# Kernel tuning notes

Hardware: AMD Instinct MI355X
Metric: run time of the kernel (lower is better)

Reference implementation:

```python
import jax, jax.numpy as jnp
import numpy as np
from jax import lax

SPARSITY = 0.5  # args.sparsity: fraction of weights KEPT


def get_subnet(scores, k):
    """GetSubnet.forward: sort |scores|, zero lowest (1-k) fraction, one elsewhere."""
    sa = jnp.abs(scores)
    n = sa.size
    j = int((1.0 - k) * n)  # static: number of entries zeroed
    idx = jnp.argsort(sa.ravel())  # ascending, matches torch .sort()
    mask = jnp.zeros((n,), dtype=sa.dtype).at[idx[j:]].set(1.0)
    return mask.reshape(scores.shape)


def masked_conv(x, w, s, b, stride):
    m = get_subnet(s, SPARSITY)
    y = lax.conv_general_dilated(
        x, w * m, window_strides=(stride, stride), padding=((1, 1), (1, 1)),
        dimension_numbers=('NCHW', 'OIHW', 'NCHW'))
    return y + b[None, :, None, None]


def setup_inputs() -> dict:
    key = jax.random.key(0)
    ks = jax.random.split(key, 16)
    def rn(k, shape, scale):
        return jax.random.normal(k, shape, dtype=jnp.float32) * scale
    return {
        'x':   rn(ks[0], (64, 3, 64, 64), 1.0),
        'w1':  rn(ks[1], (128, 3, 3, 3), 0.2),   's1': rn(ks[2], (128, 3, 3, 3), 1.0),   'b1': rn(ks[3], (128,), 0.01),
        'w2':  rn(ks[4], (256, 128, 3, 3), 0.05), 's2': rn(ks[5], (256, 128, 3, 3), 1.0), 'b2': rn(ks[6], (256,), 0.01),
        'w3':  rn(ks[7], (512, 256, 3, 3), 0.03), 's3': rn(ks[8], (512, 256, 3, 3), 1.0), 'b3': rn(ks[9], (512,), 0.01),
        'fw1': rn(ks[10], (1024, 512), 0.05),     'fs1': rn(ks[11], (1024, 512), 1.0),    'fb1': rn(ks[12], (1024,), 0.01),
        'fw2': rn(ks[13], (10, 1024), 0.05),      'fs2': rn(ks[14], (10, 1024), 1.0),     'fb2': rn(ks[15], (10,), 0.01),
    }


def reference(x, w1, s1, b1, w2, s2, b2, w3, s3, b3, fw1, fs1, fb1, fw2, fs2, fb2):
    h = jax.nn.relu(masked_conv(x, w1, s1, b1, stride=1))   # [64,128,64,64]
    h = jax.nn.relu(masked_conv(h, w2, s2, b2, stride=2))   # [64,256,32,32]
    h = jax.nn.relu(masked_conv(h, w3, s3, b3, stride=2))   # [64,512,16,16]
    h = h.mean(axis=(2, 3))                                 # [64,512] global avg pool
    m1 = get_subnet(fs1, SPARSITY)
    h = jax.nn.relu(h @ (fw1 * m1).T + fb1)                 # [64,1024]
    m2 = get_subnet(fs2, SPARSITY)
    return h @ (fw2 * m2).T + fb2                           # [64,10]
```

## Files before the change

### kernel.cpp

```cpp
#include <hip/hip_runtime.h>
#include <stdint.h>


typedef __attribute__((ext_vector_type(8))) short short8;
typedef __attribute__((ext_vector_type(4))) short short4v;
typedef __attribute__((ext_vector_type(4))) float floatx4;

__device__ __forceinline__ unsigned short f2bf(float f) {
    unsigned u = __float_as_uint(f);
    u += 0x7fffu + ((u >> 16) & 1u);
    return (unsigned short)(u >> 16);
}

constexpr unsigned CUM0 = 3456u;
constexpr unsigned CUM1 = 298368u;
constexpr unsigned CUM2 = 1478016u;
constexpr unsigned CUM3 = 2002304u;
constexpr unsigned STOT = 2012544u;
constexpr int NBH = 512;

__device__ __forceinline__ int find_tensor(unsigned idx, unsigned& li) {
    if (idx < CUM0) { li = idx;        return 0; }
    if (idx < CUM1) { li = idx - CUM0; return 1; }
    if (idx < CUM2) { li = idx - CUM1; return 2; }
    if (idx < CUM3) { li = idx - CUM2; return 3; }
    li = idx - CUM3; return 4;
}

__global__ __launch_bounds__(256) void hist11(const float* __restrict__ s0,
                                              const float* __restrict__ s1,
                                              const float* __restrict__ s2,
                                              const float* __restrict__ s3,
                                              const float* __restrict__ s4,
                                              const unsigned* __restrict__ P,
                                              unsigned* __restrict__ ghist, int pass) {
    __shared__ unsigned lh[10240];
    const int tid = threadIdx.x;
    const int NB = (pass == 2) ? 512 : 2048;
    for (int i = tid; i < NB * 5; i += 256) lh[i] = 0;
    __syncthreads();

    unsigned pref[5];
    #pragma unroll
    for (int t = 0; t < 5; t++) pref[t] = pass ? P[t] : 0u;
    const int fsh = (pass == 1) ? 20 : 9;

    for (unsigned idx = blockIdx.x * 256u + tid; idx < STOT; idx += NBH * 256u) {
        unsigned li; int t = find_tensor(idx, li);
        const float* sp = t == 0 ? s0 : t == 1 ? s1 : t == 2 ? s2 : t == 3 ? s3 : s4;
        unsigned key = __float_as_uint(sp[li]) & 0x7fffffffu;
        bool ok = (pass == 0) || ((key >> fsh) == pref[t]);
        if (ok) {
            unsigned bin = (pass == 0) ? (key >> 20)
                         : (pass == 1) ? ((key >> 9) & 2047u)
                                       : (key & 511u);
            atomicAdd(&lh[(unsigned)t * NB + bin], 1u);
        }
    }
    __syncthreads();
    const int goff = (pass == 0) ? 0 : (pass == 1) ? 10240 : 20480;
    for (int i = tid; i < NB * 5; i += 256) {
        unsigned v = lh[i];
        if (v) atomicAdd(&ghist[goff + i], v);
    }
}

__global__ __launch_bounds__(256) void find11(const unsigned* __restrict__ ghist,
                                              unsigned* __restrict__ P,
                                              unsigned* __restrict__ targ, int pass) {
    const int t = blockIdx.x;
    const int tid = threadIdx.x;
    const int NB = (pass == 2) ? 512 : 2048;
    const int goff = (pass == 0) ? 0 : (pass == 1) ? 10240 : 20480;
    const int seg = NB / 256;
    __shared__ unsigned bins[2048];
    __shared__ unsigned part[256];
    for (int i = tid; i < NB; i += 256) bins[i] = ghist[goff + t * NB + i];
    __syncthreads();
    unsigned s = 0;
    for (int j = 0; j < seg; j++) s += bins[tid * seg + j];
    part[tid] = s;
    __syncthreads();
    if (tid == 0) {
        unsigned n = t == 0 ? 3456u : t == 1 ? 294912u : t == 2 ? 1179648u
                   : t == 3 ? 524288u : 10240u;
        unsigned target = (pass == 0) ? (n >> 1) : targ[t];
        unsigned cum = 0; int q = 0;
        for (; q < 256; q++) { unsigned c = part[q]; if (cum + c > target) break; cum += c; }
        int b = q * seg;
        for (;; b++) { unsigned c = bins[b]; if (cum + c > target) break; cum += c; }
        targ[t] = target - cum;
        if (pass == 0)      P[t] = (unsigned)b;
        else if (pass == 1) P[t] = (P[t] << 11) | (unsigned)b;
        else                P[t] = (P[t] << 9) | (unsigned)b;
    }
}

__global__ void mask_reorder(const float* __restrict__ w0, const float* __restrict__ w1,
                             const float* __restrict__ w2, const float* __restrict__ w3,
                             const float* __restrict__ w4,
                             const float* __restrict__ s0, const float* __restrict__ s1,
                             const float* __restrict__ s2, const float* __restrict__ s3,
                             const float* __restrict__ s4,
                             const unsigned* __restrict__ T,
                             float* __restrict__ wm1,
                             unsigned short* __restrict__ A2,
                             unsigned short* __restrict__ A3,
                             float* __restrict__ fwm1, float* __restrict__ fwm2,
                             float* __restrict__ pooled) {
    unsigned idx = blockIdx.x * 256u + threadIdx.x;
    if (idx >= STOT) return;
    if (idx < 32768u) pooled[idx] = 0.f;
    unsigned li; int t = find_tensor(idx, li);
    const float* sp = t == 0 ? s0 : t == 1 ? s1 : t == 2 ? s2 : t == 3 ? s3 : s4;
    const float* wp = t == 0 ? w0 : t == 1 ? w1 : t == 2 ? w2 : t == 3 ? w3 : w4;
    unsigned key = __float_as_uint(sp[li]) & 0x7fffffffu;
    float val = (key >= T[t]) ? wp[li] : 0.f;
    if (t == 0) {
        wm1[li] = val;
    } else if (t == 1) {
        unsigned k = li / 1152u, r = li - k * 1152u;
        unsigned c = r / 9u, e = r - c * 9u;
        A2[((size_t)e * 256u + k) * 128u + c] = f2bf(val);
    } else if (t == 2) {
        unsigned k = li / 2304u, r = li - k * 2304u;
        unsigned c = r / 9u, e = r - c * 9u;
        A3[((size_t)e * 512u + k) * 256u + c] = f2bf(val);
    } else if (t == 3) {
        fwm1[li] = val;
    } else {
        fwm2[li] = val;
    }
}

template <int C, int H, int W, int K, int TX, int TY, int KT>
__global__ __launch_bounds__(TX* TY) void conv_direct(const float* __restrict__ in,
                                                      const float* __restrict__ wm,
                                                      const float* __restrict__ bias,
                                                      unsigned short* __restrict__ out) {
    constexpr int TILW = TX * 2, TILH = TY * 2;
    constexpr int ITW = TILW + 2, ITH = TILH + 2;
    constexpr int NTHREADS = TX * TY;
    constexpr int NLOAD = (ITH * ITW + NTHREADS - 1) / NTHREADS;
    constexpr int KG = K / KT;

    __shared__ float sIn[ITH * ITW];
    __shared__ float sW[9 * KT];

    const int tid = threadIdx.x;
    const int tx = tid % TX, ty = tid / TX;
    const int kg = blockIdx.z % KG, n = blockIdx.z / KG;
    const int ox0 = blockIdx.x * TILW, oy0 = blockIdx.y * TILH;
    const int ix0 = ox0 - 1, iy0 = oy0 - 1;

    const float* inN = in + (size_t)n * C * H * W;
    const float* wkg = wm + (size_t)kg * KT * C * 9;

    int goff[NLOAD];
    #pragma unroll
    for (int i = 0; i < NLOAD; i++) {
        int idx = tid + i * NTHREADS;
        if (idx < ITH * ITW) {
            int r = idx / ITW, col = idx % ITW;
            int gy = iy0 + r, gx = ix0 + col;
            goff[i] = (gy >= 0 && gy < H && gx >= 0 && gx < W) ? (gy * W + gx) : -1;
        } else goff[i] = -2;
    }

    float acc[2][2][KT];
    #pragma unroll
    for (int py = 0; py < 2; py++)
        #pragma unroll
        for (int px = 0; px < 2; px++)
            #pragma unroll
            for (int j = 0; j < KT; j++) acc[py][px][j] = 0.f;

    for (int c = 0; c < C; c++) {
        const float* inC = inN + (size_t)c * H * W;
        #pragma unroll
        for (int i = 0; i < NLOAD; i++) {
            int g = goff[i];
            if (g >= -1) sIn[tid + i * NTHREADS] = (g >= 0) ? inC[g] : 0.f;
        }
        for (int i = tid; i < 9 * KT; i += NTHREADS) {
            int e = i / KT, j = i % KT;
            sW[i] = wkg[j * C * 9 + c * 9 + e];
        }
        __syncthreads();

        float vin[4][4];
        const float* base = &sIn[(ty * 2) * ITW + tx * 2];
        #pragma unroll
        for (int r = 0; r < 4; r++)
            #pragma unroll
            for (int cc = 0; cc < 4; cc++) vin[r][cc] = base[r * ITW + cc];

        #pragma unroll
        for (int e = 0; e < 9; e++) {
            const int dy = e / 3, dx = e % 3;
            #pragma unroll
            for (int j = 0; j < KT; j++) {
                float wv = sW[e * KT + j];
                #pragma unroll
                for (int py = 0; py < 2; py++)
                    #pragma unroll
                    for (int px = 0; px < 2; px++)
                        acc[py][px][j] = fmaf(vin[py + dy][px + dx], wv, acc[py][px][j]);
            }
        }
        __syncthreads();
    }

    float bj[KT];
    #pragma unroll
    for (int j = 0; j < KT; j++) bj[j] = bias[kg * KT + j];
    #pragma unroll
    for (int py = 0; py < 2; py++)
        #pragma unroll
        for (int px = 0; px < 2; px++) {
            int oy = oy0 + ty * 2 + py, ox = ox0 + tx * 2 + px;
            short8 v;
            #pragma unroll
            for (int j = 0; j < KT; j++) {
                float t = acc[py][px][j] + bj[j];
                v[j] = (short)f2bf(t > 0.f ? t : 0.f);
            }
            *(short8*)(out + ((size_t)(n * H + oy) * W + ox) * K + kg * KT) = v;
        }
}

template <int C, int H, int W, int KOUT, bool POOL>
__global__ __launch_bounds__(256) void conv_mfma(const unsigned short* __restrict__ in,
                                                 const unsigned short* __restrict__ A,
                                                 const float* __restrict__ bias,
                                                 void* __restrict__ outv) {
    constexpr int OH = H / 2, OW = W / 2;
    constexpr int PR = 128 / OW;
    constexpr int RH = 2 * PR + 1;
    constexpr int IW = W + 1;
    constexpr int NC = C / 32;
    constexpr int PSTR = 40;
    constexpr int NSLOT = RH * IW * 4;
    constexpr int SLMAX = (NSLOT + 255) / 256;

    __shared__ unsigned short sIn[RH * IW * PSTR];

    const int tid = threadIdx.x;
    const int lane = tid & 63;
    const int wv = tid >> 6;
    const int l15 = lane & 15;
    const int quad = lane >> 4;
    const int pt = blockIdx.x, kb = blockIdx.y, n = blockIdx.z;
    const int k0 = kb * 128;
    const int oy0 = pt * PR;
    const int g0y = 2 * oy0 - 1;
    const int mw = wv * 32;

    int goff[SLMAX], slds[SLMAX];
    #pragma unroll
    for (int i = 0; i < SLMAX; i++) {
        int s = tid + i * 256;
        if (s < NSLOT) {
            int q = s & 3, pix = s >> 2;
            int ix = pix % IW, iy = pix / IW;
            int gy = g0y + iy, gx = ix - 1;
            slds[i] = pix * PSTR + q * 8;
            goff[i] = (gy >= 0 && gy < H && gx >= 0) ? ((gy * W + gx) * C + q * 8) : -1;
        } else { goff[i] = -2; slds[i] = 0; }
    }

    int pB[8];
    #pragma unroll
    for (int fn = 0; fn < 8; fn++) {
        int p = fn * 16 + l15;
        int oyl = p / OW, oxl = p % OW;
        pB[fn] = (oyl * 2 * IW + oxl * 2) * PSTR + quad * 8;
    }

    const unsigned short* inN = in + (size_t)n * H * W * C;

    floatx4 acc[2][8];
    #pragma unroll
    for (int fm = 0; fm < 2; fm++)
        #pragma unroll
        for (int fn = 0; fn < 8; fn++) acc[fm][fn] = (floatx4){0.f, 0.f, 0.f, 0.f};

    for (int cc = 0; cc < NC; cc++) {
        __syncthreads();
        const int cof = cc * 32;
        #pragma unroll
        for (int i = 0; i < SLMAX; i++) {
            int g = goff[i];
            if (g >= 0) {
                *(short8*)&sIn[slds[i]] = *(const short8*)(inN + g + cof);
            } else if (g == -1 && cc == 0) {
                *(short8*)&sIn[slds[i]] = (short8){0, 0, 0, 0, 0, 0, 0, 0};
            }
        }
        __syncthreads();

        const unsigned short* Abase = A + (size_t)(k0 + mw + l15) * C + cof + quad * 8;
        const size_t estr = (size_t)KOUT * C;

        short8 a0 = *(const short8*)(Abase);
        short8 a1 = *(const short8*)(Abase + 16 * C);

        #pragma unroll 1
        for (int e = 0; e < 9; e++) {
            short8 ac0 = a0, ac1 = a1;
            if (e < 8) {
                a0 = *(const short8*)(Abase + (size_t)(e + 1) * estr);
                a1 = *(const short8*)(Abase + (size_t)(e + 1) * estr + 16 * C);
            }
            const int dy = e / 3, dx = e - dy * 3;
            const int boff = (dy * IW + dx) * PSTR;
            short8 bfr[8];
            #pragma unroll
            for (int fn = 0; fn < 8; fn++)
                bfr[fn] = *(const short8*)&sIn[pB[fn] + boff];
            #pragma unroll
            for (int fn = 0; fn < 8; fn++) {
                acc[0][fn] = __builtin_amdgcn_mfma_f32_16x16x32_bf16(ac0, bfr[fn], acc[0][fn], 0, 0, 0);
                acc[1][fn] = __builtin_amdgcn_mfma_f32_16x16x32_bf16(ac1, bfr[fn], acc[1][fn], 0, 0, 0);
            }
        }
    }

    if (!POOL) {
        unsigned short* out = (unsigned short*)outv;
        #pragma unroll
        for (int fm = 0; fm < 2; fm++) {
            const int k4 = k0 + mw + fm * 16 + quad * 4;
            float b0 = bias[k4], b1 = bias[k4 + 1], b2 = bias[k4 + 2], b3 = bias[k4 + 3];
            #pragma unroll
            for (int fn = 0; fn < 8; fn++) {
                int p = fn * 16 + l15;
                int oy = oy0 + p / OW, ox = p % OW;
                float v0 = acc[fm][fn][0] + b0, v1 = acc[fm][fn][1] + b1;
                float v2 = acc[fm][fn][2] + b2, v3 = acc[fm][fn][3] + b3;
                short4v v;
                v[0] = (short)f2bf(v0 > 0.f ? v0 : 0.f);
                v[1] = (short)f2bf(v1 > 0.f ? v1 : 0.f);
                v[2] = (short)f2bf(v2 > 0.f ? v2 : 0.f);
                v[3] = (short)f2bf(v3 > 0.f ? v3 : 0.f);
                *(short4v*)(out + ((size_t)(n * OH + oy) * OW + ox) * KOUT + k4) = v;
            }
        }
    } else {
        float* out = (float*)outv;
        #pragma unroll
        for (int fm = 0; fm < 2; fm++) {
            #pragma unroll
            for (int reg = 0; reg < 4; reg++) {
                int k = k0 + mw + fm * 16 + quad * 4 + reg;
                float bv = bias[k];
                float s = 0.f;
                #pragma unroll
                for (int fn = 0; fn < 8; fn++) {
                    float v = acc[fm][fn][reg] + bv;
                    s += v > 0.f ? v : 0.f;
                }
                s += __shfl_xor(s, 1); s += __shfl_xor(s, 2);
                s += __shfl_xor(s, 4); s += __shfl_xor(s, 8);
                if (l15 == 0) atomicAdd(&out[n * KOUT + k], s * (1.0f / (OH * OW)));
            }
        }
    }
}

__global__ void fc1_kernel(const float* __restrict__ pooled, const float* __restrict__ w,
                           const float* __restrict__ b, float* __restrict__ out) {
    int t = blockIdx.x * 256 + threadIdx.x;
    int o = t & 1023, n = t >> 10;
    const float4* w4 = (const float4*)(w + (size_t)o * 512);
    const float4* p4 = (const float4*)(pooled + (size_t)n * 512);
    float acc = 0.f;
    for (int i = 0; i < 128; i++) {
        float4 a = p4[i], ww = w4[i];
        acc += a.x * ww.x + a.y * ww.y + a.z * ww.z + a.w * ww.w;
    }
    acc += b[o];
    out[t] = acc > 0.f ? acc : 0.f;
}

__global__ void fc2_kernel(const float* __restrict__ h, const float* __restrict__ w,
                           const float* __restrict__ b, float* __restrict__ out) {
    int n = blockIdx.x, tid = threadIdx.x;
    __shared__ float redw[40];
    const float4* h4 = (const float4*)(h + (size_t)n * 1024);
    float4 a = h4[tid];
    for (int o = 0; o < 10; o++) {
        const float4* w4 = (const float4*)(w + (size_t)o * 1024);
        float4 ww = w4[tid];
        float v = a.x * ww.x + a.y * ww.y + a.z * ww.z + a.w * ww.w;
        for (int off = 32; off > 0; off >>= 1) v += __shfl_down(v, off);
        if ((tid & 63) == 0) redw[o * 4 + (tid >> 6)] = v;
    }
    __syncthreads();
    if (tid < 10) {
        float s = redw[tid * 4] + redw[tid * 4 + 1] + redw[tid * 4 + 2] + redw[tid * 4 + 3] + b[tid];
        out[n * 10 + tid] = s;
    }
}

extern "C" void kernel_launch(void* const* d_in, const int* in_sizes, int n_in,
                              void* d_out, int out_size, void* d_ws, size_t ws_size,
                              hipStream_t stream) {
    const float* x   = (const float*)d_in[0];
    const float* w1  = (const float*)d_in[1];
    const float* s1  = (const float*)d_in[2];
    const float* b1  = (const float*)d_in[3];
    const float* w2  = (const float*)d_in[4];
    const float* s2  = (const float*)d_in[5];
    const float* b2  = (const float*)d_in[6];
    const float* w3  = (const float*)d_in[7];
    const float* s3  = (const float*)d_in[8];
    const float* b3  = (const float*)d_in[9];
    const float* fw1 = (const float*)d_in[10];
    const float* fs1 = (const float*)d_in[11];
    const float* fb1 = (const float*)d_in[12];
    const float* fw2 = (const float*)d_in[13];
    const float* fs2 = (const float*)d_in[14];
    const float* fb2 = (const float*)d_in[15];
    float* out = (float*)d_out;

    char* ws = (char*)d_ws;
    size_t off = 0;
    auto alloc = [&](size_t bytes) -> char* {
        char* p = ws + off;
        off = (off + bytes + 255) & ~(size_t)255;
        return p;
    };
    unsigned* ghist = (unsigned*)alloc(23040ull * 4);
    unsigned* P     = (unsigned*)alloc(64);
    unsigned* targ  = (unsigned*)alloc(64);
    float* wm1  = (float*)alloc(3456ull * 4);
    float* fwm1 = (float*)alloc(524288ull * 4);
    float* fwm2 = (float*)alloc(10240ull * 4);
    unsigned short* A2 = (unsigned short*)alloc(294912ull * 2);
    unsigned short* A3 = (unsigned short*)alloc(1179648ull * 2);
    unsigned short* h1 = (unsigned short*)alloc(33554432ull * 2);
    unsigned short* h2 = (unsigned short*)alloc(16777216ull * 2);
    float* pooled = (float*)alloc(32768ull * 4);
    float* fc1h   = (float*)alloc(65536ull * 4);
    if (off > ws_size) return;

    (void)hipMemsetAsync(ghist, 0, 23040ull * 4, stream);

    for (int pass = 0; pass < 3; pass++) {
        hist11<<<NBH, 256, 0, stream>>>(s1, s2, s3, fs1, fs2, P, ghist, pass);
        find11<<<5, 256, 0, stream>>>(ghist, P, targ, pass);
    }
    int gs = (STOT + 255) / 256;
    mask_reorder<<<gs, 256, 0, stream>>>(w1, w2, w3, fw1, fw2, s1, s2, s3, fs1, fs2, P,
                                         wm1, A2, A3, fwm1, fwm2, pooled);

    conv_direct<3, 64, 64, 128, 16, 16, 8>
        <<<dim3(2, 2, 64 * 16), 256, 0, stream>>>(x, wm1, b1, h1);
    conv_mfma<128, 64, 64, 256, false>
        <<<dim3(8, 2, 64), 256, 0, stream>>>(h1, A2, b2, h2);
    conv_mfma<256, 32, 32, 512, true>
        <<<dim3(2, 4, 64), 256, 0, stream>>>(h2, A3, b3, pooled);

    fc1_kernel<<<256, 256, 0, stream>>>(pooled, fwm1, fb1, fc1h);
    fc2_kernel<<<64, 256, 0, stream>>>(fc1h, fwm2, fb2, out);
}
```

Measured before the change: 403.1 us.

## Prefetch conv input chunks into registers and shrink MFMA pixel tiles

The two MFMA conv kernels now load the next channel chunk from global memory into registers while the current chunk is computed from shared memory. This hides global load latency behind the MFMA work. The pixel tile per block is halved from 128 to 64, which doubles the grid and cuts accumulator registers, and launch bounds now request 4 blocks per SM. Layer 3 also swaps the grid's y and z axes to change block scheduling order. The costs are an extra barrier per chunk, more register staging, and weight fragments reloaded across twice as many blocks.

```diff
diff --git a/kernel.cpp b/kernel.cpp
--- a/kernel.cpp
+++ b/kernel.cpp
@@ -229,13 +229,14 @@
         }
 }
 
-template <int C, int H, int W, int KOUT, bool POOL>
-__global__ __launch_bounds__(256) void conv_mfma(const unsigned short* __restrict__ in,
-                                                 const unsigned short* __restrict__ A,
-                                                 const float* __restrict__ bias,
-                                                 void* __restrict__ outv) {
+template <int C, int H, int W, int KOUT, int NPIX, bool POOL, bool SWAPYZ>
+__global__ __launch_bounds__(256, 4) void conv_mfma(const unsigned short* __restrict__ in,
+                                                    const unsigned short* __restrict__ A,
+                                                    const float* __restrict__ bias,
+                                                    void* __restrict__ outv) {
     constexpr int OH = H / 2, OW = W / 2;
-    constexpr int PR = 128 / OW;
+    constexpr int PR = NPIX / OW;
+    constexpr int FN = NPIX / 16;
     constexpr int RH = 2 * PR + 1;
     constexpr int IW = W + 1;
     constexpr int NC = C / 32;
@@ -250,7 +251,9 @@
     const int wv = tid >> 6;
     const int l15 = lane & 15;
     const int quad = lane >> 4;
-    const int pt = blockIdx.x, kb = blockIdx.y, n = blockIdx.z;
+    const int pt = blockIdx.x;
+    const int kb = SWAPYZ ? blockIdx.z : blockIdx.y;
+    const int n  = SWAPYZ ? blockIdx.y : blockIdx.z;
     const int k0 = kb * 128;
     const int oy0 = pt * PR;
     const int g0y = 2 * oy0 - 1;
@@ -269,9 +272,9 @@
         } else { goff[i] = -2; slds[i] = 0; }
     }
 
-    int pB[8];
-    #pragma unroll
-    for (int fn = 0; fn < 8; fn++) {
+    int pB[FN];
+    #pragma unroll
+    for (int fn = 0; fn < FN; fn++) {
         int p = fn * 16 + l15;
         int oyl = p / OW, oxl = p % OW;
         pB[fn] = (oyl * 2 * IW + oxl * 2) * PSTR + quad * 8;
@@ -279,25 +282,39 @@
 
     const unsigned short* inN = in + (size_t)n * H * W * C;
 
-    floatx4 acc[2][8];
+    floatx4 acc[2][FN];
     #pragma unroll
     for (int fm = 0; fm < 2; fm++)
         #pragma unroll
-        for (int fn = 0; fn < 8; fn++) acc[fm][fn] = (floatx4){0.f, 0.f, 0.f, 0.f};
+        for (int fn = 0; fn < FN; fn++) acc[fm][fn] = (floatx4){0.f, 0.f, 0.f, 0.f};
+
+    short8 st[SLMAX];
+    #pragma unroll
+    for (int i = 0; i < SLMAX; i++) {
+        int g = goff[i];
+        if (g >= 0) st[i] = *(const short8*)(inN + g);
+    }
 
     for (int cc = 0; cc < NC; cc++) {
-        __syncthreads();
         const int cof = cc * 32;
         #pragma unroll
         for (int i = 0; i < SLMAX; i++) {
             int g = goff[i];
             if (g >= 0) {
-                *(short8*)&sIn[slds[i]] = *(const short8*)(inN + g + cof);
+                *(short8*)&sIn[slds[i]] = st[i];
             } else if (g == -1 && cc == 0) {
                 *(short8*)&sIn[slds[i]] = (short8){0, 0, 0, 0, 0, 0, 0, 0};
             }
         }
         __syncthreads();
+        if (cc + 1 < NC) {
+            const int ncof = cof + 32;
+            #pragma unroll
+            for (int i = 0; i < SLMAX; i++) {
+                int g = goff[i];
+                if (g >= 0) st[i] = *(const short8*)(inN + g + ncof);
+            }
+        }
 
         const unsigned short* Abase = A + (size_t)(k0 + mw + l15) * C + cof + quad * 8;
         const size_t estr = (size_t)KOUT * C;
@@ -314,16 +331,17 @@
             }
             const int dy = e / 3, dx = e - dy * 3;
             const int boff = (dy * IW + dx) * PSTR;
-            short8 bfr[8];
-            #pragma unroll
-            for (int fn = 0; fn < 8; fn++)
+            short8 bfr[FN];
+            #pragma unroll
+            for (int fn = 0; fn < FN; fn++)
                 bfr[fn] = *(const short8*)&sIn[pB[fn] + boff];
             #pragma unroll
-            for (int fn = 0; fn < 8; fn++) {
+            for (int fn = 0; fn < FN; fn++) {
                 acc[0][fn] = __builtin_amdgcn_mfma_f32_16x16x32_bf16(ac0, bfr[fn], acc[0][fn], 0, 0, 0);
                 acc[1][fn] = __builtin_amdgcn_mfma_f32_16x16x32_bf16(ac1, bfr[fn], acc[1][fn], 0, 0, 0);
             }
         }
+        __syncthreads();
     }
 
     if (!POOL) {
@@ -333,7 +351,7 @@
             const int k4 = k0 + mw + fm * 16 + quad * 4;
             float b0 = bias[k4], b1 = bias[k4 + 1], b2 = bias[k4 + 2], b3 = bias[k4 + 3];
             #pragma unroll
-            for (int fn = 0; fn < 8; fn++) {
+            for (int fn = 0; fn < FN; fn++) {
                 int p = fn * 16 + l15;
                 int oy = oy0 + p / OW, ox = p % OW;
                 float v0 = acc[fm][fn][0] + b0, v1 = acc[fm][fn][1] + b1;
@@ -356,7 +374,7 @@
                 float bv = bias[k];
                 float s = 0.f;
                 #pragma unroll
-                for (int fn = 0; fn < 8; fn++) {
+                for (int fn = 0; fn < FN; fn++) {
                     float v = acc[fm][fn][reg] + bv;
                     s += v > 0.f ? v : 0.f;
                 }
@@ -457,10 +475,10 @@
 
     conv_direct<3, 64, 64, 128, 16, 16, 8>
         <<<dim3(2, 2, 64 * 16), 256, 0, stream>>>(x, wm1, b1, h1);
-    conv_mfma<128, 64, 64, 256, false>
-        <<<dim3(8, 2, 64), 256, 0, stream>>>(h1, A2, b2, h2);
-    conv_mfma<256, 32, 32, 512, true>
-        <<<dim3(2, 4, 64), 256, 0, stream>>>(h2, A3, b3, pooled);
+    conv_mfma<128, 64, 64, 256, 64, false, false>
+        <<<dim3(16, 2, 64), 256, 0, stream>>>(h1, A2, b2, h2);
+    conv_mfma<256, 32, 32, 512, 64, true, true>
+        <<<dim3(4, 64, 4), 256, 0, stream>>>(h2, A3, b3, pooled);
 
     fc1_kernel<<<256, 256, 0, stream>>>(pooled, fwm1, fb1, fc1h);
     fc2_kernel<<<64, 256, 0, stream>>>(fc1h, fwm2, fb2, out);
```

After: 424.2 us. 1.05x slower.
